# Kernel optimization log

Measured on AMD Instinct MI355X. Metric: run time of the kernel, lower is better.

## Reference

```python
import jax, jax.numpy as jnp
import numpy as np

H = 12          # num heads
D = 768         # hidden size
DH = D // H     # head dim = 64
DE = 768        # encoder hidden size


def setup_inputs() -> dict:
    key = jax.random.key(0)
    ks = jax.random.split(key, 10)
    s = 0.02
    return {
        "hidden_states": jax.random.normal(ks[0], (2, 2048, D), dtype=jnp.float32),
        "encoder_hidden_states": jax.random.normal(ks[1], (2, 4096, DE), dtype=jnp.float32),
        "Wq": jax.random.normal(ks[2], (D, D), dtype=jnp.float32) * s,
        "bq": jnp.zeros((D,), dtype=jnp.float32),
        "Wk": jax.random.normal(ks[3], (DE, D), dtype=jnp.float32) * s,
        "bk": jnp.zeros((D,), dtype=jnp.float32),
        "Wv": jax.random.normal(ks[4], (DE, D), dtype=jnp.float32) * s,
        "bv": jnp.zeros((D,), dtype=jnp.float32),
        "Wo": jax.random.normal(ks[5], (D, D), dtype=jnp.float32) * s,
        "bo": jnp.zeros((D,), dtype=jnp.float32),
    }


def _split_heads(x):
    # [B, S, D] -> [B, H, S, DH]
    B, S, _ = x.shape
    return x.reshape(B, S, H, DH).transpose(0, 2, 1, 3)


def reference(hidden_states, encoder_hidden_states, Wq, bq, Wk, bk, Wv, bv, Wo, bo):
    q = _split_heads(hidden_states @ Wq + bq)              # [B,H,Sq,DH]
    k = _split_heads(encoder_hidden_states @ Wk + bk)      # [B,H,Skv,DH]
    v = _split_heads(encoder_hidden_states @ Wv + bv)      # [B,H,Skv,DH]
    scale = 1.0 / jnp.sqrt(jnp.asarray(DH, dtype=q.dtype))
    scores = jnp.einsum("bhqd,bhkd->bhqk", q, k) * scale   # [B,H,Sq,Skv]
    probs = jax.nn.softmax(scores, axis=-1)
    ctx = jnp.einsum("bhqk,bhkd->bhqd", probs, v)          # [B,H,Sq,DH]
    B, _, Sq, _ = ctx.shape
    ctx = ctx.transpose(0, 2, 1, 3).reshape(B, Sq, D)      # [B,Sq,D]
    return ctx @ Wo + bo
```

## Files before the change

### kernel.cpp

```cpp
#include <hip/hip_runtime.h>

typedef __attribute__((ext_vector_type(8))) short bf16x8;
typedef __attribute__((ext_vector_type(4))) float f32x4;
typedef __attribute__((ext_vector_type(8))) unsigned short u16x8;
typedef __attribute__((ext_vector_type(4))) unsigned short u16x4;

static constexpr int Bsz = 2, SQ = 2048, SKV = 4096, Dm = 768, NH = 12, DH = 64;

static __device__ __forceinline__ unsigned short f2bf(float f) {
  unsigned int u = __float_as_uint(f);
  u += 0x7fff + ((u >> 16) & 1);
  return (unsigned short)(u >> 16);
}

__global__ void cvt_kernel(const float* __restrict__ in, unsigned short* __restrict__ out, int n8) {
  int i = blockIdx.x * blockDim.x + threadIdx.x;
  if (i >= n8) return;
  const float4* p = reinterpret_cast<const float4*>(in) + (size_t)i * 2;
  float4 a = p[0], b = p[1];
  u16x8 o;
  o[0] = f2bf(a.x); o[1] = f2bf(a.y); o[2] = f2bf(a.z); o[3] = f2bf(a.w);
  o[4] = f2bf(b.x); o[5] = f2bf(b.y); o[6] = f2bf(b.z); o[7] = f2bf(b.w);
  *(reinterpret_cast<u16x8*>(out) + i) = o;
}

__global__ void wtrans4(const float* __restrict__ Wq, const float* __restrict__ Wk,
                        const float* __restrict__ Wv, const float* __restrict__ Wo,
                        unsigned short* __restrict__ oq, unsigned short* __restrict__ ok,
                        unsigned short* __restrict__ ov, unsigned short* __restrict__ oo) {
  __shared__ float t[32][33];
  const int z = blockIdx.z;
  const float* W = (z == 0) ? Wq : (z == 1) ? Wk : (z == 2) ? Wv : Wo;
  unsigned short* WT = (z == 0) ? oq : (z == 1) ? ok : (z == 2) ? ov : oo;
  int n0 = blockIdx.x * 32, k0 = blockIdx.y * 32;
  int tx = threadIdx.x, ty = threadIdx.y;
  #pragma unroll
  for (int i = 0; i < 4; ++i)
    t[ty * 4 + i][tx] = W[(size_t)(k0 + ty * 4 + i) * Dm + n0 + tx];
  __syncthreads();
  #pragma unroll
  for (int i = 0; i < 4; ++i)
    WT[(size_t)(n0 + ty * 4 + i) * Dm + k0 + tx] = f2bf(t[tx][ty * 4 + i]);
}

template <int BM, int BN, bool F32OUT>
static __device__ __forceinline__ void gemm_body(const unsigned short* __restrict__ A,
                                                 const unsigned short* __restrict__ BT,
                                                 const float* __restrict__ bias,
                                                 void* __restrict__ Cout, float scale,
                                                 int row0, int col0,
                                                 unsigned short* As, unsigned short* Bs) {
  const int wave = threadIdx.x >> 6, lane = threadIdx.x & 63;
  const int wr = wave >> 1, wc = wave & 1;
  const int lrow = lane & 15, lk8 = (lane >> 4) << 3;
  constexpr int MI = BM / 32, NJ = BN / 32;
  f32x4 acc[MI][NJ] = {};

  for (int k0 = 0; k0 < Dm; k0 += 32) {
    #pragma unroll
    for (int j = 0; j < BM / 64; ++j) {
      int e = (threadIdx.x + j * 256) * 8;
      int r = e >> 5, c = e & 31;
      const unsigned short* src = A + (size_t)(row0 + r) * Dm + k0 + c;
      __builtin_amdgcn_global_load_lds((const __attribute__((address_space(1))) void*)src,
                                       (__attribute__((address_space(3))) void*)(As + e), 16, 0, 0);
    }
    #pragma unroll
    for (int j = 0; j < BN / 64; ++j) {
      int e = (threadIdx.x + j * 256) * 8;
      int r = e >> 5, c = e & 31;
      const unsigned short* src = BT + (size_t)(col0 + r) * Dm + k0 + c;
      __builtin_amdgcn_global_load_lds((const __attribute__((address_space(1))) void*)src,
                                       (__attribute__((address_space(3))) void*)(Bs + e), 16, 0, 0);
    }
    __syncthreads();
    bf16x8 a[MI], b[NJ];
    #pragma unroll
    for (int mi = 0; mi < MI; ++mi)
      a[mi] = *(const bf16x8*)&As[(wr * (BM / 2) + mi * 16 + lrow) * 32 + lk8];
    #pragma unroll
    for (int nj = 0; nj < NJ; ++nj)
      b[nj] = *(const bf16x8*)&Bs[(wc * (BN / 2) + nj * 16 + lrow) * 32 + lk8];
    #pragma unroll
    for (int mi = 0; mi < MI; ++mi)
      #pragma unroll
      for (int nj = 0; nj < NJ; ++nj)
        acc[mi][nj] = __builtin_amdgcn_mfma_f32_16x16x32_bf16(a[mi], b[nj], acc[mi][nj], 0, 0, 0);
    __syncthreads();
  }

  const int r4 = (lane >> 4) << 2;
  #pragma unroll
  for (int nj = 0; nj < NJ; ++nj) {
    int gcol = col0 + wc * (BN / 2) + nj * 16 + lrow;
    float bb = bias[gcol];
    #pragma unroll
    for (int mi = 0; mi < MI; ++mi) {
      #pragma unroll
      for (int r = 0; r < 4; ++r) {
        int grow = row0 + wr * (BM / 2) + mi * 16 + r4 + r;
        float v = (acc[mi][nj][r] + bb) * scale;
        if constexpr (F32OUT) ((float*)Cout)[(size_t)grow * Dm + gcol] = v;
        else                  ((unsigned short*)Cout)[(size_t)grow * Dm + gcol] = f2bf(v);
      }
    }
  }
}

__global__ __launch_bounds__(256) void qkv_gemm(const unsigned short* __restrict__ hsb,
                                                const unsigned short* __restrict__ ehsb,
                                                const unsigned short* __restrict__ wqt,
                                                const unsigned short* __restrict__ wkt,
                                                const unsigned short* __restrict__ wvt,
                                                const float* __restrict__ bq,
                                                const float* __restrict__ bk,
                                                const float* __restrict__ bv,
                                                unsigned short* __restrict__ qb,
                                                unsigned short* __restrict__ kb,
                                                unsigned short* __restrict__ vb) {
  __shared__ unsigned short As[128 * 32];
  __shared__ unsigned short Bs[128 * 32];
  const int tile = blockIdx.y;
  const unsigned short *A, *BT; const float* bias; unsigned short* out;
  float scale; int row0;
  if (tile < 32)      { A = hsb;  BT = wqt; bias = bq; out = qb; scale = 0.125f; row0 = tile * 128; }
  else if (tile < 96) { A = ehsb; BT = wkt; bias = bk; out = kb; scale = 1.0f;   row0 = (tile - 32) * 128; }
  else                { A = ehsb; BT = wvt; bias = bv; out = vb; scale = 1.0f;   row0 = (tile - 96) * 128; }
  gemm_body<128, 128, false>(A, BT, bias, out, scale, row0, blockIdx.x * 128, As, Bs);
}

__global__ __launch_bounds__(256) void o_gemm(const unsigned short* __restrict__ A,
                                              const unsigned short* __restrict__ BT,
                                              const float* __restrict__ bias,
                                              float* __restrict__ Cout) {
  __shared__ unsigned short As[64 * 32];
  __shared__ unsigned short Bs[64 * 32];
  gemm_body<64, 64, true>(A, BT, bias, Cout, 1.0f, blockIdx.y * 64, blockIdx.x * 64, As, Bs);
}

__global__ __launch_bounds__(256) void attn_kernel(const unsigned short* __restrict__ Q,
                                                   const unsigned short* __restrict__ K,
                                                   const unsigned short* __restrict__ V,
                                                   unsigned short* __restrict__ Ctx) {
  __shared__ unsigned short Ks[64 * 64];
  __shared__ unsigned short Vt[64 * 70];
  const int qt = blockIdx.x, h = blockIdx.y, b = blockIdx.z;
  const int wave = threadIdx.x >> 6, lane = threadIdx.x & 63;
  const int lrow = lane & 15, lg = lane >> 4, lk8 = lg << 3;
  const size_t qoff = (size_t)b * SQ * Dm + (size_t)h * DH;
  const size_t koff = (size_t)b * SKV * Dm + (size_t)h * DH;

  const int qrow = qt * 64 + wave * 16 + lrow;
  bf16x8 qa[2];
  qa[0] = *(const bf16x8*)(Q + qoff + (size_t)qrow * Dm + lk8);
  qa[1] = *(const bf16x8*)(Q + qoff + (size_t)qrow * Dm + 32 + lk8);

  f32x4 acc[4] = {};
  float m_run = -3e38f, l_run = 0.f;

  const int srow = threadIdx.x >> 2;
  const int sc0 = (threadIdx.x & 3) * 16;
  u16x8 kreg0, kreg1, vreg0, vreg1;
  {
    const unsigned short* kp = K + koff + (size_t)srow * Dm + sc0;
    const unsigned short* vp = V + koff + (size_t)srow * Dm + sc0;
    kreg0 = *(const u16x8*)kp; kreg1 = *(const u16x8*)(kp + 8);
    vreg0 = *(const u16x8*)vp; vreg1 = *(const u16x8*)(vp + 8);
  }
  unsigned short* ksw0 = Ks + srow * 64 + ((((sc0 * 2)     ) ^ ((srow & 7) << 4)) >> 1);
  unsigned short* ksw1 = Ks + srow * 64 + ((((sc0 * 2) + 16) ^ ((srow & 7) << 4)) >> 1);
  const int swz = (lrow & 7) << 4;

  constexpr int NT = SKV / 64;
  for (int kt = 0; kt < NT; ++kt) {
    __syncthreads();
    *(u16x8*)ksw0 = kreg0;
    *(u16x8*)ksw1 = kreg1;
    #pragma unroll
    for (int j = 0; j < 8; ++j) {
      Vt[(sc0 + j) * 70 + srow]     = vreg0[j];
      Vt[(sc0 + 8 + j) * 70 + srow] = vreg1[j];
    }
    __syncthreads();
    if (kt + 1 < NT) {
      const unsigned short* kp = K + koff + ((size_t)(kt + 1) * 64 + srow) * Dm + sc0;
      const unsigned short* vp = V + koff + ((size_t)(kt + 1) * 64 + srow) * Dm + sc0;
      kreg0 = *(const u16x8*)kp; kreg1 = *(const u16x8*)(kp + 8);
      vreg0 = *(const u16x8*)vp; vreg1 = *(const u16x8*)(vp + 8);
    }

    f32x4 s[4] = {};
    __builtin_amdgcn_s_setprio(1);
    #pragma unroll
    for (int ks = 0; ks < 2; ++ks)
      #pragma unroll
      for (int nj = 0; nj < 4; ++nj) {
        bf16x8 kf = *(const bf16x8*)&Ks[(nj * 16 + lrow) * 64 + (((ks * 64 + lg * 16) ^ swz) >> 1)];
        s[nj] = __builtin_amdgcn_mfma_f32_16x16x32_bf16(kf, qa[ks], s[nj], 0, 0, 0);
      }
    __builtin_amdgcn_s_setprio(0);

    float mx = -3e38f;
    #pragma unroll
    for (int nj = 0; nj < 4; ++nj)
      #pragma unroll
      for (int r = 0; r < 4; ++r) mx = fmaxf(mx, s[nj][r]);
    mx = fmaxf(mx, __shfl_xor(mx, 16));
    mx = fmaxf(mx, __shfl_xor(mx, 32));
    float mnew = fmaxf(m_run, mx);
    float alpha = __expf(m_run - mnew);
    m_run = mnew;
    float e[4][4];
    float rs = 0.f;
    #pragma unroll
    for (int nj = 0; nj < 4; ++nj)
      #pragma unroll
      for (int r = 0; r < 4; ++r) { e[nj][r] = __expf(s[nj][r] - mnew); rs += e[nj][r]; }
    rs += __shfl_xor(rs, 16);
    rs += __shfl_xor(rs, 32);
    l_run = l_run * alpha + rs;

    float alr[4];
    #pragma unroll
    for (int r = 0; r < 4; ++r) alr[r] = __shfl(alpha, (lg << 2) + r);
    #pragma unroll
    for (int dj = 0; dj < 4; ++dj)
      #pragma unroll
      for (int r = 0; r < 4; ++r) acc[dj][r] *= alr[r];

    #pragma unroll
    for (int ks = 0; ks < 2; ++ks) {
      bf16x8 pa;
      #pragma unroll
      for (int j = 0; j < 4; ++j) {
        pa[j]     = (short)f2bf(e[2 * ks][j]);
        pa[4 + j] = (short)f2bf(e[2 * ks + 1][j]);
      }
      __builtin_amdgcn_s_setprio(1);
      #pragma unroll
      for (int dj = 0; dj < 4; ++dj) {
        const int vrow = (dj * 16 + lrow) * 70 + ks * 32 + lg * 4;
        u16x4 v0 = *(const u16x4*)&Vt[vrow];
        u16x4 v1 = *(const u16x4*)&Vt[vrow + 16];
        bf16x8 vf;
        #pragma unroll
        for (int j = 0; j < 4; ++j) { vf[j] = (short)v0[j]; vf[4 + j] = (short)v1[j]; }
        acc[dj] = __builtin_amdgcn_mfma_f32_16x16x32_bf16(pa, vf, acc[dj], 0, 0, 0);
      }
      __builtin_amdgcn_s_setprio(0);
    }
  }

  float linv[4];
  #pragma unroll
  for (int r = 0; r < 4; ++r) {
    float lr = __shfl(l_run, (lg << 2) + r);
    linv[r] = 1.0f / lr;
  }
  const int qbase = qt * 64 + wave * 16;
  #pragma unroll
  for (int dj = 0; dj < 4; ++dj)
    #pragma unroll
    for (int r = 0; r < 4; ++r)
      Ctx[qoff + (size_t)(qbase + 4 * lg + r) * Dm + dj * 16 + lrow] = f2bf(acc[dj][r] * linv[r]);
}

extern "C" void kernel_launch(void* const* d_in, const int* in_sizes, int n_in,
                              void* d_out, int out_size, void* d_ws, size_t ws_size,
                              hipStream_t stream) {
  const float* hs  = (const float*)d_in[0];
  const float* ehs = (const float*)d_in[1];
  const float* Wq  = (const float*)d_in[2];
  const float* bq  = (const float*)d_in[3];
  const float* Wk  = (const float*)d_in[4];
  const float* bk  = (const float*)d_in[5];
  const float* Wv  = (const float*)d_in[6];
  const float* bv  = (const float*)d_in[7];
  const float* Wo  = (const float*)d_in[8];
  const float* bo  = (const float*)d_in[9];
  float* out = (float*)d_out;

  unsigned short* hsb  = (unsigned short*)d_ws;
  unsigned short* ehsb = hsb  + (size_t)Bsz * SQ * Dm;
  unsigned short* wqt  = ehsb + (size_t)Bsz * SKV * Dm;
  unsigned short* wkt  = wqt + (size_t)Dm * Dm;
  unsigned short* wvt  = wkt + (size_t)Dm * Dm;
  unsigned short* wot  = wvt + (size_t)Dm * Dm;
  unsigned short* qb   = wot + (size_t)Dm * Dm;
  unsigned short* kb   = qb  + (size_t)Bsz * SQ * Dm;
  unsigned short* vb   = kb  + (size_t)Bsz * SKV * Dm;
  unsigned short* ctxb = vb  + (size_t)Bsz * SKV * Dm;

  const int nHS = Bsz * SQ * Dm, nEHS = Bsz * SKV * Dm;
  cvt_kernel<<<(nHS / 8 + 255) / 256, 256, 0, stream>>>(hs, hsb, nHS / 8);
  cvt_kernel<<<(nEHS / 8 + 255) / 256, 256, 0, stream>>>(ehs, ehsb, nEHS / 8);

  wtrans4<<<dim3(24, 24, 4), dim3(32, 8), 0, stream>>>(Wq, Wk, Wv, Wo, wqt, wkt, wvt, wot);

  qkv_gemm<<<dim3(6, 160), 256, 0, stream>>>(hsb, ehsb, wqt, wkt, wvt, bq, bk, bv, qb, kb, vb);

  attn_kernel<<<dim3(SQ / 64, NH, Bsz), 256, 0, stream>>>(qb, kb, vb, ctxb);

  o_gemm<<<dim3(12, 64), 256, 0, stream>>>(ctxb, wot, bo, out);
}
```

Measured before the change: 294.8 us.

## Double-buffer GEMM and attention LDS with async loads, pre-transpose V

The GEMM body now double-buffers its LDS tiles, issuing direct global-to-LDS loads for the next k-step while MFMAs run on the current one, with one barrier per step. A new kernel transposes V into a per-head, permuted layout so attention can stream K and V tiles directly into swizzled LDS double buffers, replacing the register-staged scalar V transpose. Attention also swaps the MFMA operand order so each lane owns a query row, which removes the alpha and l shuffles and allows vectorised Ctx stores. The o_gemm tile grows to 128x64. The cost is an extra launch and a full pass over V, which reuses the ehsb workspace region as its output.

New measurement: 278.2 us. 5.6% less time.

```diff
diff --git a/kernel.cpp b/kernel.cpp
--- a/kernel.cpp
+++ b/kernel.cpp
@@ -43,6 +43,32 @@
     WT[(size_t)(n0 + ty * 4 + i) * Dm + k0 + tx] = f2bf(t[tx][ty * 4 + i]);
 }
 
+__global__ void vtrans(const unsigned short* __restrict__ vb, unsigned short* __restrict__ vtp) {
+  __shared__ unsigned short t[64][65];
+  const int kt = blockIdx.x, h = blockIdx.y, b = blockIdx.z;
+  const int tid = threadIdx.x;
+  const int kr = tid >> 2, dc = (tid & 3) * 16;
+  const unsigned short* src = vb + ((size_t)(b * SKV + kt * 64 + kr)) * Dm + h * DH + dc;
+  u16x8 a0 = *(const u16x8*)src, a1 = *(const u16x8*)(src + 8);
+  #pragma unroll
+  for (int j = 0; j < 8; ++j) { t[kr][dc + j] = a0[j]; t[kr][dc + 8 + j] = a1[j]; }
+  __syncthreads();
+  const int d = tid >> 2, p0 = (tid & 3) * 16;
+  u16x8 o0, o1;
+  #pragma unroll
+  for (int j = 0; j < 16; ++j) {
+    int pos = p0 + j;
+    int pos5 = pos & 31;
+    int kv5 = ((pos5 >> 3) & 3) * 4 + ((pos5 >> 2) & 1) * 16 + (pos5 & 3);
+    int kv = (pos & 32) | kv5;
+    unsigned short v = t[kv][d];
+    if (j < 8) o0[j] = v; else o1[j - 8] = v;
+  }
+  unsigned short* dst = vtp + ((size_t)(b * NH + h) * DH + d) * SKV + kt * 64 + p0;
+  *(u16x8*)dst = o0;
+  *(u16x8*)(dst + 8) = o1;
+}
+
 template <int BM, int BN, bool F32OUT>
 static __device__ __forceinline__ void gemm_body(const unsigned short* __restrict__ A,
                                                  const unsigned short* __restrict__ BT,
@@ -50,43 +76,54 @@
                                                  void* __restrict__ Cout, float scale,
                                                  int row0, int col0,
                                                  unsigned short* As, unsigned short* Bs) {
-  const int wave = threadIdx.x >> 6, lane = threadIdx.x & 63;
+  const int tid = threadIdx.x;
+  const int wave = tid >> 6, lane = tid & 63;
   const int wr = wave >> 1, wc = wave & 1;
   const int lrow = lane & 15, lk8 = (lane >> 4) << 3;
   constexpr int MI = BM / 32, NJ = BN / 32;
+  constexpr int AG = BM / 64, BG = BN / 64;
+  constexpr int KS = Dm / 32;
   f32x4 acc[MI][NJ] = {};
 
-  for (int k0 = 0; k0 < Dm; k0 += 32) {
-    #pragma unroll
-    for (int j = 0; j < BM / 64; ++j) {
-      int e = (threadIdx.x + j * 256) * 8;
-      int r = e >> 5, c = e & 31;
-      const unsigned short* src = A + (size_t)(row0 + r) * Dm + k0 + c;
-      __builtin_amdgcn_global_load_lds((const __attribute__((address_space(1))) void*)src,
-                                       (__attribute__((address_space(3))) void*)(As + e), 16, 0, 0);
-    }
-    #pragma unroll
-    for (int j = 0; j < BN / 64; ++j) {
-      int e = (threadIdx.x + j * 256) * 8;
-      int r = e >> 5, c = e & 31;
-      const unsigned short* src = BT + (size_t)(col0 + r) * Dm + k0 + c;
-      __builtin_amdgcn_global_load_lds((const __attribute__((address_space(1))) void*)src,
-                                       (__attribute__((address_space(3))) void*)(Bs + e), 16, 0, 0);
-    }
-    __syncthreads();
+  auto stage = [&](int buf, int k0) {
+    #pragma unroll
+    for (int j = 0; j < AG; ++j) {
+      int e = (tid + j * 256) * 8; int r = e >> 5, c = e & 31;
+      __builtin_amdgcn_global_load_lds(
+          (const __attribute__((address_space(1))) void*)(A + (size_t)(row0 + r) * Dm + k0 + c),
+          (__attribute__((address_space(3))) void*)(As + buf * (BM * 32) + e), 16, 0, 0);
+    }
+    #pragma unroll
+    for (int j = 0; j < BG; ++j) {
+      int e = (tid + j * 256) * 8; int r = e >> 5, c = e & 31;
+      __builtin_amdgcn_global_load_lds(
+          (const __attribute__((address_space(1))) void*)(BT + (size_t)(col0 + r) * Dm + k0 + c),
+          (__attribute__((address_space(3))) void*)(Bs + buf * (BN * 32) + e), 16, 0, 0);
+    }
+  };
+
+  stage(0, 0);
+  asm volatile("s_waitcnt vmcnt(0)" ::: "memory");
+  __builtin_amdgcn_s_barrier();
+  for (int ki = 0; ki < KS; ++ki) {
+    const int buf = ki & 1;
+    if (ki + 1 < KS) stage(buf ^ 1, (ki + 1) * 32);
     bf16x8 a[MI], b[NJ];
     #pragma unroll
     for (int mi = 0; mi < MI; ++mi)
-      a[mi] = *(const bf16x8*)&As[(wr * (BM / 2) + mi * 16 + lrow) * 32 + lk8];
+      a[mi] = *(const bf16x8*)&As[buf * (BM * 32) + (wr * (BM / 2) + mi * 16 + lrow) * 32 + lk8];
     #pragma unroll
     for (int nj = 0; nj < NJ; ++nj)
-      b[nj] = *(const bf16x8*)&Bs[(wc * (BN / 2) + nj * 16 + lrow) * 32 + lk8];
+      b[nj] = *(const bf16x8*)&Bs[buf * (BN * 32) + (wc * (BN / 2) + nj * 16 + lrow) * 32 + lk8];
     #pragma unroll
     for (int mi = 0; mi < MI; ++mi)
       #pragma unroll
       for (int nj = 0; nj < NJ; ++nj)
         acc[mi][nj] = __builtin_amdgcn_mfma_f32_16x16x32_bf16(a[mi], b[nj], acc[mi][nj], 0, 0, 0);
-    __syncthreads();
+    if (ki + 1 < KS) {
+      asm volatile("s_waitcnt vmcnt(0)" ::: "memory");
+      __builtin_amdgcn_s_barrier();
+    }
   }
 
   const int r4 = (lane >> 4) << 2;
@@ -118,8 +155,8 @@
                                                 unsigned short* __restrict__ qb,
                                                 unsigned short* __restrict__ kb,
                                                 unsigned short* __restrict__ vb) {
-  __shared__ unsigned short As[128 * 32];
-  __shared__ unsigned short Bs[128 * 32];
+  __shared__ unsigned short As[2 * 128 * 32];
+  __shared__ unsigned short Bs[2 * 128 * 32];
   const int tile = blockIdx.y;
   const unsigned short *A, *BT; const float* bias; unsigned short* out;
   float scale; int row0;
@@ -133,61 +170,66 @@
                                               const unsigned short* __restrict__ BT,
                                               const float* __restrict__ bias,
                                               float* __restrict__ Cout) {
-  __shared__ unsigned short As[64 * 32];
-  __shared__ unsigned short Bs[64 * 32];
-  gemm_body<64, 64, true>(A, BT, bias, Cout, 1.0f, blockIdx.y * 64, blockIdx.x * 64, As, Bs);
+  __shared__ unsigned short As[2 * 128 * 32];
+  __shared__ unsigned short Bs[2 * 64 * 32];
+  gemm_body<128, 64, true>(A, BT, bias, Cout, 1.0f, blockIdx.y * 128, blockIdx.x * 64, As, Bs);
 }
 
 __global__ __launch_bounds__(256) void attn_kernel(const unsigned short* __restrict__ Q,
                                                    const unsigned short* __restrict__ K,
-                                                   const unsigned short* __restrict__ V,
+                                                   const unsigned short* __restrict__ VT,
                                                    unsigned short* __restrict__ Ctx) {
-  __shared__ unsigned short Ks[64 * 64];
-  __shared__ unsigned short Vt[64 * 70];
+  __shared__ unsigned short Ks[2][64 * 64];
+  __shared__ unsigned short Vs[2][64 * 64];
   const int qt = blockIdx.x, h = blockIdx.y, b = blockIdx.z;
-  const int wave = threadIdx.x >> 6, lane = threadIdx.x & 63;
+  const int tid = threadIdx.x;
+  const int wave = tid >> 6, lane = tid & 63;
   const int lrow = lane & 15, lg = lane >> 4, lk8 = lg << 3;
   const size_t qoff = (size_t)b * SQ * Dm + (size_t)h * DH;
   const size_t koff = (size_t)b * SKV * Dm + (size_t)h * DH;
+  const size_t voff = (size_t)(b * NH + h) * DH * SKV;
 
   const int qrow = qt * 64 + wave * 16 + lrow;
-  bf16x8 qa[2];
-  qa[0] = *(const bf16x8*)(Q + qoff + (size_t)qrow * Dm + lk8);
-  qa[1] = *(const bf16x8*)(Q + qoff + (size_t)qrow * Dm + 32 + lk8);
+  const bf16x8 qa0 = *(const bf16x8*)(Q + qoff + (size_t)qrow * Dm + lk8);
+  const bf16x8 qa1 = *(const bf16x8*)(Q + qoff + (size_t)qrow * Dm + 32 + lk8);
+
+  const unsigned short* ksrc[2];
+  const unsigned short* vsrc[2];
+  int dste[2];
+  #pragma unroll
+  for (int c = 0; c < 2; ++c) {
+    int db = (tid + c * 256) * 16;
+    int r = db >> 7, cb = db & 127;
+    int sc = (cb ^ ((r & 7) << 4)) >> 1;
+    ksrc[c] = K + koff + (size_t)r * Dm + sc;
+    vsrc[c] = VT + voff + (size_t)r * SKV + sc;
+    dste[c] = db >> 1;
+  }
+
+  auto stage = [&](int buf, int kt) {
+    #pragma unroll
+    for (int c = 0; c < 2; ++c) {
+      __builtin_amdgcn_global_load_lds(
+          (const __attribute__((address_space(1))) void*)(ksrc[c] + (size_t)kt * 64 * Dm),
+          (__attribute__((address_space(3))) void*)(&Ks[buf][dste[c]]), 16, 0, 0);
+      __builtin_amdgcn_global_load_lds(
+          (const __attribute__((address_space(1))) void*)(vsrc[c] + kt * 64),
+          (__attribute__((address_space(3))) void*)(&Vs[buf][dste[c]]), 16, 0, 0);
+    }
+  };
 
   f32x4 acc[4] = {};
   float m_run = -3e38f, l_run = 0.f;
-
-  const int srow = threadIdx.x >> 2;
-  const int sc0 = (threadIdx.x & 3) * 16;
-  u16x8 kreg0, kreg1, vreg0, vreg1;
-  {
-    const unsigned short* kp = K + koff + (size_t)srow * Dm + sc0;
-    const unsigned short* vp = V + koff + (size_t)srow * Dm + sc0;
-    kreg0 = *(const u16x8*)kp; kreg1 = *(const u16x8*)(kp + 8);
-    vreg0 = *(const u16x8*)vp; vreg1 = *(const u16x8*)(vp + 8);
-  }
-  unsigned short* ksw0 = Ks + srow * 64 + ((((sc0 * 2)     ) ^ ((srow & 7) << 4)) >> 1);
-  unsigned short* ksw1 = Ks + srow * 64 + ((((sc0 * 2) + 16) ^ ((srow & 7) << 4)) >> 1);
   const int swz = (lrow & 7) << 4;
+
+  stage(0, 0);
+  asm volatile("s_waitcnt vmcnt(0)" ::: "memory");
+  __builtin_amdgcn_s_barrier();
 
   constexpr int NT = SKV / 64;
   for (int kt = 0; kt < NT; ++kt) {
-    __syncthreads();
-    *(u16x8*)ksw0 = kreg0;
-    *(u16x8*)ksw1 = kreg1;
-    #pragma unroll
-    for (int j = 0; j < 8; ++j) {
-      Vt[(sc0 + j) * 70 + srow]     = vreg0[j];
-      Vt[(sc0 + 8 + j) * 70 + srow] = vreg1[j];
-    }
-    __syncthreads();
-    if (kt + 1 < NT) {
-      const unsigned short* kp = K + koff + ((size_t)(kt + 1) * 64 + srow) * Dm + sc0;
-      const unsigned short* vp = V + koff + ((size_t)(kt + 1) * 64 + srow) * Dm + sc0;
-      kreg0 = *(const u16x8*)kp; kreg1 = *(const u16x8*)(kp + 8);
-      vreg0 = *(const u16x8*)vp; vreg1 = *(const u16x8*)(vp + 8);
-    }
+    const int buf = kt & 1;
+    if (kt + 1 < NT) stage(buf ^ 1, kt + 1);
 
     f32x4 s[4] = {};
     __builtin_amdgcn_s_setprio(1);
@@ -195,8 +237,9 @@
     for (int ks = 0; ks < 2; ++ks)
       #pragma unroll
       for (int nj = 0; nj < 4; ++nj) {
-        bf16x8 kf = *(const bf16x8*)&Ks[(nj * 16 + lrow) * 64 + (((ks * 64 + lg * 16) ^ swz) >> 1)];
-        s[nj] = __builtin_amdgcn_mfma_f32_16x16x32_bf16(kf, qa[ks], s[nj], 0, 0, 0);
+        const int cb = (ks * 64 + lg * 16) ^ swz;
+        bf16x8 kf = *(const bf16x8*)((const char*)&Ks[buf][0] + (nj * 16 + lrow) * 128 + cb);
+        s[nj] = __builtin_amdgcn_mfma_f32_16x16x32_bf16(kf, ks ? qa1 : qa0, s[nj], 0, 0, 0);
       }
     __builtin_amdgcn_s_setprio(0);
 
@@ -207,8 +250,8 @@
       for (int r = 0; r < 4; ++r) mx = fmaxf(mx, s[nj][r]);
     mx = fmaxf(mx, __shfl_xor(mx, 16));
     mx = fmaxf(mx, __shfl_xor(mx, 32));
-    float mnew = fmaxf(m_run, mx);
-    float alpha = __expf(m_run - mnew);
+    const float mnew = fmaxf(m_run, mx);
+    const float alpha = __expf(m_run - mnew);
     m_run = mnew;
     float e[4][4];
     float rs = 0.f;
@@ -219,14 +262,10 @@
     rs += __shfl_xor(rs, 16);
     rs += __shfl_xor(rs, 32);
     l_run = l_run * alpha + rs;
-
-    float alr[4];
-    #pragma unroll
-    for (int r = 0; r < 4; ++r) alr[r] = __shfl(alpha, (lg << 2) + r);
     #pragma unroll
     for (int dj = 0; dj < 4; ++dj)
       #pragma unroll
-      for (int r = 0; r < 4; ++r) acc[dj][r] *= alr[r];
+      for (int r = 0; r < 4; ++r) acc[dj][r] *= alpha;
 
     #pragma unroll
     for (int ks = 0; ks < 2; ++ks) {
@@ -239,30 +278,27 @@
       __builtin_amdgcn_s_setprio(1);
       #pragma unroll
       for (int dj = 0; dj < 4; ++dj) {
-        const int vrow = (dj * 16 + lrow) * 70 + ks * 32 + lg * 4;
-        u16x4 v0 = *(const u16x4*)&Vt[vrow];
-        u16x4 v1 = *(const u16x4*)&Vt[vrow + 16];
-        bf16x8 vf;
-        #pragma unroll
-        for (int j = 0; j < 4; ++j) { vf[j] = (short)v0[j]; vf[4 + j] = (short)v1[j]; }
-        acc[dj] = __builtin_amdgcn_mfma_f32_16x16x32_bf16(pa, vf, acc[dj], 0, 0, 0);
+        const int cb = (ks * 64 + lg * 16) ^ swz;
+        bf16x8 vf = *(const bf16x8*)((const char*)&Vs[buf][0] + (dj * 16 + lrow) * 128 + cb);
+        acc[dj] = __builtin_amdgcn_mfma_f32_16x16x32_bf16(vf, pa, acc[dj], 0, 0, 0);
       }
       __builtin_amdgcn_s_setprio(0);
     }
-  }
-
-  float linv[4];
-  #pragma unroll
-  for (int r = 0; r < 4; ++r) {
-    float lr = __shfl(l_run, (lg << 2) + r);
-    linv[r] = 1.0f / lr;
-  }
-  const int qbase = qt * 64 + wave * 16;
-  #pragma unroll
-  for (int dj = 0; dj < 4; ++dj)
-    #pragma unroll
-    for (int r = 0; r < 4; ++r)
-      Ctx[qoff + (size_t)(qbase + 4 * lg + r) * Dm + dj * 16 + lrow] = f2bf(acc[dj][r] * linv[r]);
+
+    if (kt + 1 < NT) {
+      asm volatile("s_waitcnt vmcnt(0)" ::: "memory");
+      __builtin_amdgcn_s_barrier();
+    }
+  }
+
+  const float linv = 1.0f / l_run;
+  #pragma unroll
+  for (int dj = 0; dj < 4; ++dj) {
+    u16x4 o;
+    #pragma unroll
+    for (int r = 0; r < 4; ++r) o[r] = f2bf(acc[dj][r] * linv);
+    *(u16x4*)(Ctx + qoff + (size_t)qrow * Dm + dj * 16 + (lg << 2)) = o;
+  }
 }
 
 extern "C" void kernel_launch(void* const* d_in, const int* in_sizes, int n_in,
@@ -290,6 +326,7 @@
   unsigned short* kb   = qb  + (size_t)Bsz * SQ * Dm;
   unsigned short* vb   = kb  + (size_t)Bsz * SKV * Dm;
   unsigned short* ctxb = vb  + (size_t)Bsz * SKV * Dm;
+  unsigned short* vtp  = ehsb;
 
   const int nHS = Bsz * SQ * Dm, nEHS = Bsz * SKV * Dm;
   cvt_kernel<<<(nHS / 8 + 255) / 256, 256, 0, stream>>>(hs, hsb, nHS / 8);
@@ -299,7 +336,9 @@
 
   qkv_gemm<<<dim3(6, 160), 256, 0, stream>>>(hsb, ehsb, wqt, wkt, wvt, bq, bk, bv, qb, kb, vb);
 
-  attn_kernel<<<dim3(SQ / 64, NH, Bsz), 256, 0, stream>>>(qb, kb, vb, ctxb);
-
-  o_gemm<<<dim3(12, 64), 256, 0, stream>>>(ctxb, wot, bo, out);
-}
+  vtrans<<<dim3(SKV / 64, NH, Bsz), 256, 0, stream>>>(vb, vtp);
+
+  attn_kernel<<<dim3(SQ / 64, NH, Bsz), 256, 0, stream>>>(qb, kb, vtp, ctxb);
+
+  o_gemm<<<dim3(12, 32), 256, 0, stream>>>(ctxb, wot, bo, out);
+}
```
